# Kernel optimization log

Measured on AMD Instinct MI355X. Metric: run time of the kernel, lower is better.

Reference implementation:

```python
import jax, jax.numpy as jnp
import numpy as np

N_USERS = 100000
N_ITEMS = 50000
EMB_DIM = 64
N_LAYERS = 2
N_INTENTS = 128
N_EDGES = 4000000
N_NODES = N_USERS + N_ITEMS


def setup_inputs() -> dict:
    key = jax.random.key(0)
    k1, k2, k3, k4, k5 = jax.random.split(key, 5)
    return {
        "user_emb": 0.1 * jax.random.normal(k1, (N_USERS, EMB_DIM), dtype=jnp.float32),
        "item_emb": 0.1 * jax.random.normal(k2, (N_ITEMS, EMB_DIM), dtype=jnp.float32),
        "intents": jax.random.normal(k3, (EMB_DIM, N_INTENTS), dtype=jnp.float32) * (2.0 / (EMB_DIM + N_INTENTS)) ** 0.5,
        "h_idx": jax.random.randint(k4, (N_EDGES,), 0, N_NODES, dtype=jnp.int64)
        if jax.config.jax_enable_x64 else jax.random.randint(k4, (N_EDGES,), 0, N_NODES, dtype=jnp.int32),
        "t_idx": jax.random.randint(k5, (N_EDGES,), 0, N_NODES, dtype=jnp.int32),
    }


def _spmm(h_idx, t_idx, g_vals, x):
    # y[h] += g_vals * x[t]  (sparse matrix @ dense, COO form)
    gathered = x[t_idx] * g_vals[:, None]  # [E, D]
    return jax.ops.segment_sum(gathered, h_idx, num_segments=N_NODES)


def reference(user_emb, item_emb, intents, h_idx, t_idx):
    # --- _cal_sparse_adj: G = D^{-1/2} A D^{-1/2}, A values are ones ---
    deg = jax.ops.segment_sum(jnp.ones_like(h_idx, dtype=user_emb.dtype), h_idx,
                              num_segments=N_NODES)
    d_inv_sqrt = jnp.where(deg > 0, jax.lax.rsqrt(jnp.maximum(deg, 1e-12)), 0.0)
    g_vals = d_inv_sqrt[h_idx] * d_inv_sqrt[t_idx]  # [E]

    # --- multi-layer propagation with intent-aware embeddings ---
    embs = jnp.concatenate([user_emb, item_emb], axis=0)  # [N, D]
    all_embs = [embs]
    for _ in range(N_LAYERS):
        gnn_embs = _spmm(h_idx, t_idx, g_vals, embs)  # [N, D]
        # intent projection: softmax over intents, reconstruct in emb space
        u, it = embs[:N_USERS], embs[N_USERS:]
        u_int = jax.nn.softmax(u @ intents, axis=1) @ intents.T      # [n_users, D]
        i_int = jax.nn.softmax(it @ intents, axis=1) @ intents.T     # [n_items, D]
        int_embs = jnp.concatenate([u_int, i_int], axis=0)
        embs = gnn_embs + int_embs
        all_embs.append(embs)
    out = jnp.sum(jnp.stack(all_embs, axis=1), axis=1) / len(all_embs)  # mean over layers
    return out
```

## Files before the change

### kernel.cpp

```cpp
#include <hip/hip_runtime.h>
#include <math.h>

#define N_USERS 100000
#define N_ITEMS 50000
#define N_NODES 150000
#define EMB 64
#define NI 128
#define NUM_EDGES 4000000
#define NPAD 150016
#define NB 1172
#define BSTRIDE 4352
#define ETILE 8192
#define EGRID ((NUM_EDGES + ETILE - 1) / ETILE)
#define NT_ALL (NPAD / 16)
#define SBLK (NT_ALL / 4)
#define SENT 150000u

typedef __attribute__((ext_vector_type(8))) short bf16x8;
typedef __attribute__((ext_vector_type(4))) float f32x4;

__device__ __forceinline__ unsigned short f2bf(float f) {
    unsigned int u = __float_as_uint(f);
    u += 0x7FFFu + ((u >> 16) & 1u);
    return (unsigned short)(u >> 16);
}
__device__ __forceinline__ float bflo(unsigned int u) { return __uint_as_float(u << 16); }
__device__ __forceinline__ float bfhi(unsigned int u) { return __uint_as_float(u & 0xFFFF0000u); }


__global__ __launch_bounds__(512) void bucket_scatter(const int* __restrict__ h,
                                                      const int* __restrict__ t,
                                                      int* __restrict__ gcur,
                                                      unsigned int* __restrict__ ebuf) {
    __shared__ int lc[NB];
    __shared__ int lbase[NB];
    __shared__ int lcur[NB];
    int tid = threadIdx.x;
    for (int i = tid; i < NB; i += 512) lc[i] = 0;
    __syncthreads();
    int base = blockIdx.x * ETILE;
#pragma unroll
    for (int k = 0; k < ETILE / 512; ++k) {
        int idx = base + k * 512 + tid;
        if (idx < NUM_EDGES) atomicAdd(&lc[h[idx] >> 7], 1);
    }
    __syncthreads();
    for (int i = tid; i < NB; i += 512) {
        int c = lc[i];
        lbase[i] = c ? (i * BSTRIDE + atomicAdd(&gcur[i], c)) : 0;
        lcur[i] = 0;
    }
    __syncthreads();
#pragma unroll
    for (int k = 0; k < ETILE / 512; ++k) {
        int idx = base + k * 512 + tid;
        if (idx < NUM_EDGES) {
            int hh = h[idx], tt = t[idx];
            int b = hh >> 7;
            int p = lbase[b] + atomicAdd(&lcur[b], 1);
            int lim = b * BSTRIDE + BSTRIDE - 1;
            p = (p <= lim) ? p : lim;
            ebuf[p] = ((unsigned int)(hh & 127) << 18) | (unsigned int)tt;
        }
    }
}


__global__ __launch_bounds__(512) void bucket_csr(const int* __restrict__ gcur,
                                                  unsigned int* __restrict__ ebuf,
                                                  int2* __restrict__ rmeta,
                                                  float* __restrict__ dinv) {
    __shared__ unsigned int in_s[BSTRIDE];
    __shared__ int cnt_s[128];
    __shared__ int base_s[128];
    __shared__ int sc[128];
    int b = blockIdx.x, tid = threadIdx.x;
    int s = b * BSTRIDE;
    int n = gcur[b];
    if (n > BSTRIDE) n = BSTRIDE;

    for (int i = tid; i < n; i += 512) in_s[i] = ebuf[s + i];
    if (tid < 128) cnt_s[tid] = 0;
    __syncthreads();
    for (int i = tid; i < n; i += 512) atomicAdd(&cnt_s[in_s[i] >> 18], 1);
    __syncthreads();

    int c = 0, pc = 0;
    if (tid < 128) {
        c = cnt_s[tid];
        pc = (c + 3) & ~3;
        sc[tid] = pc;
    }
    __syncthreads();
    for (int off = 1; off < 128; off <<= 1) {
        int tv = 0;
        if (tid < 128 && tid >= off) tv = sc[tid - off];
        __syncthreads();
        if (tid < 128 && tid >= off) sc[tid] += tv;
        __syncthreads();
    }
    if (tid < 128) {
        int excl = sc[tid] - pc;
        base_s[tid] = excl;
        int node = (b << 7) + tid;
        rmeta[node] = make_int2(s + excl, pc);
        dinv[node] = (c > 0) ? rsqrtf((float)c) : 0.0f;
        for (int p2 = c; p2 < pc; ++p2) ebuf[s + excl + p2] = SENT;
        cnt_s[tid] = 0;
    }
    __syncthreads();
    for (int i = tid; i < n; i += 512) {
        unsigned int qv = in_s[i];
        int hl = (int)(qv >> 18);
        int p = base_s[hl] + atomicAdd(&cnt_s[hl], 1);
        ebuf[s + p] = qv & 0x3FFFFu;
    }
}


__global__ void init_kernel(const float4* __restrict__ ue4, const float4* __restrict__ ie4,
                            uint2* __restrict__ ebf4, float4* __restrict__ out4) {
    int i = blockIdx.x * blockDim.x + threadIdx.x;
    const int uelems = N_USERS * EMB / 4;
    const int relems = N_NODES * EMB / 4;
    const int total  = NPAD * EMB / 4;
    if (i < total) {
        float4 v = make_float4(0.f, 0.f, 0.f, 0.f);
        if (i < uelems) v = ue4[i];
        else if (i < relems) v = ie4[i - uelems];
        if (i < relems) out4[i] = v;
        unsigned int p0 = ((unsigned int)f2bf(v.y) << 16) | f2bf(v.x);
        unsigned int p1 = ((unsigned int)f2bf(v.w) << 16) | f2bf(v.z);
        ebf4[i] = make_uint2(p0, p1);
    }
}


__global__ __launch_bounds__(256) void wconv(const float* __restrict__ W,
                                             unsigned short* __restrict__ Wt,
                                             unsigned short* __restrict__ W2b) {
    int i = blockIdx.x * 256 + threadIdx.x;
    if (i < EMB * NI) {
        int d = i >> 7, c = i & 127;
        unsigned short b = f2bf(W[i]);
        W2b[i] = b;
        Wt[c * EMB + d] = b;
    }
}


__global__ __launch_bounds__(256, 6) void spmm_intent(const int2* __restrict__ rmeta,
                                                      const unsigned int* __restrict__ col,
                                                      const float* __restrict__ dinv,
                                                      const unsigned short* __restrict__ ebf,
                                                      unsigned short* __restrict__ ebfout,
                                                      const unsigned short* __restrict__ Wt,
                                                      const unsigned short* __restrict__ W2b,
                                                      float* __restrict__ acc, float scale) {
    __shared__ __align__(16) float UPool[4][1408];

    int tid = threadIdx.x;
    int wid = tid >> 6, lane = tid & 63;
    int q = lane >> 4, c = lane & 15;
    int qq = lane >> 3, cc = lane & 7;
    int tile = blockIdx.x * 4 + wid;
    if (tile >= NT_ALL) return;
    int rowbase = tile << 4;
    float* fw = &UPool[wid][0];
    unsigned short* pw = (unsigned short*)&UPool[wid][1088];

#pragma unroll 1
    for (int half = 0; half < 2; ++half) {
        int row = rowbase + half * 8 + qq;
        int2 rm = rmeta[row];
        int s = rm.x, pcv = rm.y;
        float dr = dinv[row];

        float a0 = 0.f, a1 = 0.f, a2 = 0.f, a3 = 0.f;
        float a4 = 0.f, a5 = 0.f, a6 = 0.f, a7 = 0.f;
        const unsigned short* eb = ebf + (cc << 3);

        uint4 cg0 = *(const uint4*)&col[s];
        int e0 = (int)(cg0.x & 0x3FFFFu), e1 = (int)(cg0.y & 0x3FFFFu);
        int e2 = (int)(cg0.z & 0x3FFFFu), e3 = (int)(cg0.w & 0x3FFFFu);
        float g0 = dinv[e0], g1 = dinv[e1], g2 = dinv[e2], g3 = dinv[e3];
        uint4 u0 = *(const uint4*)(eb + ((size_t)e0 << 6));
        uint4 u1 = *(const uint4*)(eb + ((size_t)e1 << 6));
        uint4 u2 = *(const uint4*)(eb + ((size_t)e2 << 6));
        uint4 u3 = *(const uint4*)(eb + ((size_t)e3 << 6));
        uint4 cg1 = *(const uint4*)&col[s + ((pcv >= 8) ? 4 : 0)];
        int f0 = (int)(cg1.x & 0x3FFFFu), f1 = (int)(cg1.y & 0x3FFFFu);
        int f2 = (int)(cg1.z & 0x3FFFFu), f3 = (int)(cg1.w & 0x3FFFFu);

        for (int it = 0; it < pcv; it += 4) {
            float h0 = dinv[f0], h1 = dinv[f1], h2 = dinv[f2], h3 = dinv[f3];
            uint4 v0 = *(const uint4*)(eb + ((size_t)f0 << 6));
            uint4 v1 = *(const uint4*)(eb + ((size_t)f1 << 6));
            uint4 v2 = *(const uint4*)(eb + ((size_t)f2 << 6));
            uint4 v3 = *(const uint4*)(eb + ((size_t)f3 << 6));
            int cb = s + it + 8;
            int ce = s + pcv - 4;
            uint4 cgn = *(const uint4*)&col[(cb < ce) ? cb : ce];
            __builtin_amdgcn_sched_barrier(0);
            a0 = fmaf(g0, bflo(u0.x), a0); a1 = fmaf(g0, bfhi(u0.x), a1);
            a2 = fmaf(g0, bflo(u0.y), a2); a3 = fmaf(g0, bfhi(u0.y), a3);
            a4 = fmaf(g0, bflo(u0.z), a4); a5 = fmaf(g0, bfhi(u0.z), a5);
            a6 = fmaf(g0, bflo(u0.w), a6); a7 = fmaf(g0, bfhi(u0.w), a7);
            a0 = fmaf(g1, bflo(u1.x), a0); a1 = fmaf(g1, bfhi(u1.x), a1);
            a2 = fmaf(g1, bflo(u1.y), a2); a3 = fmaf(g1, bfhi(u1.y), a3);
            a4 = fmaf(g1, bflo(u1.z), a4); a5 = fmaf(g1, bfhi(u1.z), a5);
            a6 = fmaf(g1, bflo(u1.w), a6); a7 = fmaf(g1, bfhi(u1.w), a7);
            a0 = fmaf(g2, bflo(u2.x), a0); a1 = fmaf(g2, bfhi(u2.x), a1);
            a2 = fmaf(g2, bflo(u2.y), a2); a3 = fmaf(g2, bfhi(u2.y), a3);
            a4 = fmaf(g2, bflo(u2.z), a4); a5 = fmaf(g2, bfhi(u2.z), a5);
            a6 = fmaf(g2, bflo(u2.w), a6); a7 = fmaf(g2, bfhi(u2.w), a7);
            a0 = fmaf(g3, bflo(u3.x), a0); a1 = fmaf(g3, bfhi(u3.x), a1);
            a2 = fmaf(g3, bflo(u3.y), a2); a3 = fmaf(g3, bfhi(u3.y), a3);
            a4 = fmaf(g3, bflo(u3.z), a4); a5 = fmaf(g3, bfhi(u3.z), a5);
            a6 = fmaf(g3, bflo(u3.w), a6); a7 = fmaf(g3, bfhi(u3.w), a7);
            u0 = v0; u1 = v1; u2 = v2; u3 = v3;
            g0 = h0; g1 = h1; g2 = h2; g3 = h3;
            f0 = (int)(cgn.x & 0x3FFFFu); f1 = (int)(cgn.y & 0x3FFFFu);
            f2 = (int)(cgn.z & 0x3FFFFu); f3 = (int)(cgn.w & 0x3FFFFu);
        }
        int fb = (half * 8 + qq) * 68 + (cc << 3);
        fw[fb + 0] = a0 * dr; fw[fb + 1] = a1 * dr;
        fw[fb + 2] = a2 * dr; fw[fb + 3] = a3 * dr;
        fw[fb + 4] = a4 * dr; fw[fb + 5] = a5 * dr;
        fw[fb + 6] = a6 * dr; fw[fb + 7] = a7 * dr;
    }

    const unsigned short* erow = ebf + ((size_t)(rowbase + c) << 6);
    bf16x8 A0 = *(const bf16x8*)(erow + (q << 3));
    bf16x8 A1 = *(const bf16x8*)(erow + 32 + (q << 3));
    f32x4 S[8];
#pragma unroll
    for (int t = 0; t < 8; ++t) {
        bf16x8 B0 = *(const bf16x8*)&Wt[(16 * t + c) * EMB + (q << 3)];
        bf16x8 B1 = *(const bf16x8*)&Wt[(16 * t + c) * EMB + 32 + (q << 3)];
        f32x4 z = {0.f, 0.f, 0.f, 0.f};
        z = __builtin_amdgcn_mfma_f32_16x16x32_bf16(A0, B0, z, 0, 0, 0);
        S[t] = __builtin_amdgcn_mfma_f32_16x16x32_bf16(A1, B1, z, 0, 0, 0);
    }

#pragma unroll
    for (int r = 0; r < 4; ++r) {
        float m = S[0][r];
#pragma unroll
        for (int t = 1; t < 8; ++t) m = fmaxf(m, S[t][r]);
        m = fmaxf(m, __shfl_xor(m, 1)); m = fmaxf(m, __shfl_xor(m, 2));
        m = fmaxf(m, __shfl_xor(m, 4)); m = fmaxf(m, __shfl_xor(m, 8));
        float sum = 0.f;
#pragma unroll
        for (int t = 0; t < 8; ++t) { float ex = __expf(S[t][r] - m); S[t][r] = ex; sum += ex; }
        sum += __shfl_xor(sum, 1); sum += __shfl_xor(sum, 2);
        sum += __shfl_xor(sum, 4); sum += __shfl_xor(sum, 8);
        float inv = 1.0f / sum;
#pragma unroll
        for (int t = 0; t < 8; ++t) S[t][r] *= inv;
    }

    f32x4 O0 = {0.f, 0.f, 0.f, 0.f}, O1 = O0, O2 = O0, O3 = O0;
#pragma unroll
    for (int s2 = 0; s2 < 4; ++s2) {
#pragma unroll
        for (int h2 = 0; h2 < 2; ++h2) {
            int t = 2 * s2 + h2;
#pragma unroll
            for (int r = 0; r < 4; ++r) {
                float p = S[t][r];
                unsigned short b = f2bf(p);
                pw[(4 * q + r) * 40 + (h2 << 4) + c] = b;
                S[t][r] = p - bflo((unsigned int)b);
            }
        }
        bf16x8 Pf = *(const bf16x8*)&pw[c * 40 + (q << 3)];
        {
            bf16x8 Bf0 = *(const bf16x8*)&W2b[(c) * NI + (s2 << 5) + (q << 3)];
            bf16x8 Bf1 = *(const bf16x8*)&W2b[(16 + c) * NI + (s2 << 5) + (q << 3)];
            O0 = __builtin_amdgcn_mfma_f32_16x16x32_bf16(Pf, Bf0, O0, 0, 0, 0);
            O1 = __builtin_amdgcn_mfma_f32_16x16x32_bf16(Pf, Bf1, O1, 0, 0, 0);
            bf16x8 Bf2 = *(const bf16x8*)&W2b[(32 + c) * NI + (s2 << 5) + (q << 3)];
            bf16x8 Bf3 = *(const bf16x8*)&W2b[(48 + c) * NI + (s2 << 5) + (q << 3)];
            O2 = __builtin_amdgcn_mfma_f32_16x16x32_bf16(Pf, Bf2, O2, 0, 0, 0);
            O3 = __builtin_amdgcn_mfma_f32_16x16x32_bf16(Pf, Bf3, O3, 0, 0, 0);
        }
#pragma unroll
        for (int h2 = 0; h2 < 2; ++h2) {
            int t = 2 * s2 + h2;
#pragma unroll
            for (int r = 0; r < 4; ++r)
                pw[(4 * q + r) * 40 + (h2 << 4) + c] = f2bf(S[t][r]);
        }
        bf16x8 Pl = *(const bf16x8*)&pw[c * 40 + (q << 3)];
        {
            bf16x8 Bf0 = *(const bf16x8*)&W2b[(c) * NI + (s2 << 5) + (q << 3)];
            bf16x8 Bf1 = *(const bf16x8*)&W2b[(16 + c) * NI + (s2 << 5) + (q << 3)];
            O0 = __builtin_amdgcn_mfma_f32_16x16x32_bf16(Pl, Bf0, O0, 0, 0, 0);
            O1 = __builtin_amdgcn_mfma_f32_16x16x32_bf16(Pl, Bf1, O1, 0, 0, 0);
            bf16x8 Bf2 = *(const bf16x8*)&W2b[(32 + c) * NI + (s2 << 5) + (q << 3)];
            bf16x8 Bf3 = *(const bf16x8*)&W2b[(48 + c) * NI + (s2 << 5) + (q << 3)];
            O2 = __builtin_amdgcn_mfma_f32_16x16x32_bf16(Pl, Bf2, O2, 0, 0, 0);
            O3 = __builtin_amdgcn_mfma_f32_16x16x32_bf16(Pl, Bf3, O3, 0, 0, 0);
        }
    }

    asm volatile("" ::: "memory");

#pragma unroll
    for (int r = 0; r < 4; ++r) {
        int rl = 4 * q + r;
        float* gr = &fw[rl * 68];
        gr[c]      += O0[r];
        gr[16 + c] += O1[r];
        gr[32 + c] += O2[r];
        gr[48 + c] += O3[r];
    }

    {
        int j = lane >> 2, sg = lane & 3;
        int rw = rowbase + j;
        const float* gr = &fw[j * 68 + (sg << 4)];
        float4 x0 = *(const float4*)&gr[0];
        float4 x1 = *(const float4*)&gr[4];
        float4 x2 = *(const float4*)&gr[8];
        float4 x3 = *(const float4*)&gr[12];
        size_t base = ((size_t)rw << 6) + (sg << 4);
        uint4 w0, w1;
        w0.x = (unsigned int)f2bf(x0.x) | ((unsigned int)f2bf(x0.y) << 16);
        w0.y = (unsigned int)f2bf(x0.z) | ((unsigned int)f2bf(x0.w) << 16);
        w0.z = (unsigned int)f2bf(x1.x) | ((unsigned int)f2bf(x1.y) << 16);
        w0.w = (unsigned int)f2bf(x1.z) | ((unsigned int)f2bf(x1.w) << 16);
        w1.x = (unsigned int)f2bf(x2.x) | ((unsigned int)f2bf(x2.y) << 16);
        w1.y = (unsigned int)f2bf(x2.z) | ((unsigned int)f2bf(x2.w) << 16);
        w1.z = (unsigned int)f2bf(x3.x) | ((unsigned int)f2bf(x3.y) << 16);
        w1.w = (unsigned int)f2bf(x3.z) | ((unsigned int)f2bf(x3.w) << 16);
        *(uint4*)(ebfout + base) = w0;
        *(uint4*)(ebfout + base + 8) = w1;
        if (rw < N_NODES) {
            float4* ap = (float4*)(acc + base);
            float4 b0 = ap[0], b1 = ap[1], b2 = ap[2], b3 = ap[3];
            b0.x = (b0.x + x0.x) * scale; b0.y = (b0.y + x0.y) * scale;
            b0.z = (b0.z + x0.z) * scale; b0.w = (b0.w + x0.w) * scale;
            b1.x = (b1.x + x1.x) * scale; b1.y = (b1.y + x1.y) * scale;
            b1.z = (b1.z + x1.z) * scale; b1.w = (b1.w + x1.w) * scale;
            b2.x = (b2.x + x2.x) * scale; b2.y = (b2.y + x2.y) * scale;
            b2.z = (b2.z + x2.z) * scale; b2.w = (b2.w + x2.w) * scale;
            b3.x = (b3.x + x3.x) * scale; b3.y = (b3.y + x3.y) * scale;
            b3.z = (b3.z + x3.z) * scale; b3.w = (b3.w + x3.w) * scale;
            ap[0] = b0; ap[1] = b1; ap[2] = b2; ap[3] = b3;
        }
    }
}


extern "C" void kernel_launch(void* const* d_in, const int* in_sizes, int n_in,
                              void* d_out, int out_size, void* d_ws, size_t ws_size,
                              hipStream_t stream) {
    const float* ue = (const float*)d_in[0];
    const float* ie = (const float*)d_in[1];
    const float* W  = (const float*)d_in[2];
    const int*   h  = (const int*)d_in[3];
    const int*   t  = (const int*)d_in[4];
    float* out = (float*)d_out;

    int*            gcur  = (int*)d_ws;
    int2*           rmeta = (int2*)(gcur + 2048);
    float*          dinv  = (float*)(rmeta + NPAD);
    unsigned short* ebfA  = (unsigned short*)(dinv + NPAD);
    unsigned short* ebfB  = ebfA + (size_t)NPAD * EMB;
    unsigned int*   ebuf  = (unsigned int*)(ebfB + (size_t)NPAD * EMB);
    unsigned short* Wt    = (unsigned short*)(ebuf + NB * BSTRIDE + 16);
    unsigned short* W2b   = Wt + EMB * NI;

    hipMemsetAsync(gcur, 0, NB * sizeof(int), stream);
    hipMemsetAsync(ebuf + NB * BSTRIDE, 0, 16 * sizeof(unsigned int), stream);
    bucket_scatter<<<EGRID, 512, 0, stream>>>(h, t, gcur, ebuf);
    bucket_csr<<<NB, 512, 0, stream>>>(gcur, ebuf, rmeta, dinv);
    init_kernel<<<(NPAD * EMB / 4 + 255) / 256, 256, 0, stream>>>(
        (const float4*)ue, (const float4*)ie, (uint2*)ebfA, (float4*)out);
    wconv<<<(EMB * NI + 255) / 256, 256, 0, stream>>>(W, Wt, W2b);

    const unsigned int* col = ebuf;
    spmm_intent<<<SBLK, 256, 0, stream>>>(rmeta, col, dinv, ebfA, ebfB, Wt, W2b, out, 1.0f);
    spmm_intent<<<SBLK, 256, 0, stream>>>(rmeta, col, dinv, ebfB, ebfA, Wt, W2b, out, 1.0f / 3.0f);
}
```

Before: 458.2 us.

## Stage neighbor indices and degree weights in LDS; per-wave bucket counters

The SpMM gather now loads up to 64 column indices per row into shared memory cooperatively across the 8 lanes of each row group. It also precomputes their dinv weights there with padding masked to zero, then issues 8 independent row gathers per iteration instead of the software-pipelined 4-wide loop. Rows with more than 64 entries fall back to a direct loop. The CSR bucket kernel splits its shared-memory histogram into per-wave copies to reduce atomic contention. Shared memory per block grows and the occupancy hint drops from 6 to 4 blocks, which trades latency hiding for wider per-thread memory-level parallelism.

Result: faster. 443.2 us (-3.3%).

```diff
diff --git a/kernel.cpp b/kernel.cpp
--- a/kernel.cpp
+++ b/kernel.cpp
@@ -71,23 +71,27 @@
                                                   int2* __restrict__ rmeta,
                                                   float* __restrict__ dinv) {
     __shared__ unsigned int in_s[BSTRIDE];
-    __shared__ int cnt_s[128];
+    __shared__ int cnt8[8][128];
+    __shared__ int wb8[8][128];
     __shared__ int base_s[128];
     __shared__ int sc[128];
-    int b = blockIdx.x, tid = threadIdx.x;
+    int b = blockIdx.x, tid = threadIdx.x, wid = tid >> 6;
     int s = b * BSTRIDE;
     int n = gcur[b];
     if (n > BSTRIDE) n = BSTRIDE;
 
     for (int i = tid; i < n; i += 512) in_s[i] = ebuf[s + i];
-    if (tid < 128) cnt_s[tid] = 0;
-    __syncthreads();
-    for (int i = tid; i < n; i += 512) atomicAdd(&cnt_s[in_s[i] >> 18], 1);
+    for (int i = tid; i < 1024; i += 512) ((int*)cnt8)[i] = 0;
+    __syncthreads();
+    for (int i = tid; i < n; i += 512) atomicAdd(&cnt8[wid][in_s[i] >> 18], 1);
     __syncthreads();
 
     int c = 0, pc = 0;
     if (tid < 128) {
-        c = cnt_s[tid];
+        int acc = 0;
+#pragma unroll
+        for (int w = 0; w < 8; ++w) { wb8[w][tid] = acc; acc += cnt8[w][tid]; }
+        c = acc;
         pc = (c + 3) & ~3;
         sc[tid] = pc;
     }
@@ -106,13 +110,14 @@
         rmeta[node] = make_int2(s + excl, pc);
         dinv[node] = (c > 0) ? rsqrtf((float)c) : 0.0f;
         for (int p2 = c; p2 < pc; ++p2) ebuf[s + excl + p2] = SENT;
-        cnt_s[tid] = 0;
-    }
+    }
+    __syncthreads();
+    for (int i = tid; i < 1024; i += 512) ((int*)cnt8)[i] = 0;
     __syncthreads();
     for (int i = tid; i < n; i += 512) {
         unsigned int qv = in_s[i];
         int hl = (int)(qv >> 18);
-        int p = base_s[hl] + atomicAdd(&cnt_s[hl], 1);
+        int p = base_s[hl] + wb8[wid][hl] + atomicAdd(&cnt8[wid][hl], 1);
         ebuf[s + p] = qv & 0x3FFFFu;
     }
 }
@@ -149,7 +154,7 @@
 }
 
 
-__global__ __launch_bounds__(256, 6) void spmm_intent(const int2* __restrict__ rmeta,
+__global__ __launch_bounds__(256, 4) void spmm_intent(const int2* __restrict__ rmeta,
                                                       const unsigned int* __restrict__ col,
                                                       const float* __restrict__ dinv,
                                                       const unsigned short* __restrict__ ebf,
@@ -157,7 +162,7 @@
                                                       const unsigned short* __restrict__ Wt,
                                                       const unsigned short* __restrict__ W2b,
                                                       float* __restrict__ acc, float scale) {
-    __shared__ __align__(16) float UPool[4][1408];
+    __shared__ __align__(16) float UPool[4][2496];
 
     int tid = threadIdx.x;
     int wid = tid >> 6, lane = tid & 63;
@@ -168,6 +173,8 @@
     int rowbase = tile << 4;
     float* fw = &UPool[wid][0];
     unsigned short* pw = (unsigned short*)&UPool[wid][1088];
+    unsigned int* cb = (unsigned int*)&UPool[wid][1408];
+    float* gb = &UPool[wid][1952];
 
 #pragma unroll 1
     for (int half = 0; half < 2; ++half) {
@@ -176,32 +183,93 @@
         int s = rm.x, pcv = rm.y;
         float dr = dinv[row];
 
+        {
+            int eoff = cc << 3;
+            uint4 c0 = *(const uint4*)&col[s + eoff];
+            uint4 c1 = *(const uint4*)&col[s + eoff + 4];
+            c0.x = (c0.x < NPAD) ? c0.x : (NPAD - 1);
+            c0.y = (c0.y < NPAD) ? c0.y : (NPAD - 1);
+            c0.z = (c0.z < NPAD) ? c0.z : (NPAD - 1);
+            c0.w = (c0.w < NPAD) ? c0.w : (NPAD - 1);
+            c1.x = (c1.x < NPAD) ? c1.x : (NPAD - 1);
+            c1.y = (c1.y < NPAD) ? c1.y : (NPAD - 1);
+            c1.z = (c1.z < NPAD) ? c1.z : (NPAD - 1);
+            c1.w = (c1.w < NPAD) ? c1.w : (NPAD - 1);
+            int lb = qq * 68 + eoff;
+            *(uint4*)&cb[lb]     = c0;
+            *(uint4*)&cb[lb + 4] = c1;
+            float g0 = dinv[c0.x], g1 = dinv[c0.y], g2 = dinv[c0.z], g3 = dinv[c0.w];
+            float g4 = dinv[c1.x], g5 = dinv[c1.y], g6 = dinv[c1.z], g7 = dinv[c1.w];
+            gb[lb + 0] = (eoff + 0 < pcv) ? g0 : 0.f;
+            gb[lb + 1] = (eoff + 1 < pcv) ? g1 : 0.f;
+            gb[lb + 2] = (eoff + 2 < pcv) ? g2 : 0.f;
+            gb[lb + 3] = (eoff + 3 < pcv) ? g3 : 0.f;
+            gb[lb + 4] = (eoff + 4 < pcv) ? g4 : 0.f;
+            gb[lb + 5] = (eoff + 5 < pcv) ? g5 : 0.f;
+            gb[lb + 6] = (eoff + 6 < pcv) ? g6 : 0.f;
+            gb[lb + 7] = (eoff + 7 < pcv) ? g7 : 0.f;
+        }
+
         float a0 = 0.f, a1 = 0.f, a2 = 0.f, a3 = 0.f;
         float a4 = 0.f, a5 = 0.f, a6 = 0.f, a7 = 0.f;
         const unsigned short* eb = ebf + (cc << 3);
-
-        uint4 cg0 = *(const uint4*)&col[s];
-        int e0 = (int)(cg0.x & 0x3FFFFu), e1 = (int)(cg0.y & 0x3FFFFu);
-        int e2 = (int)(cg0.z & 0x3FFFFu), e3 = (int)(cg0.w & 0x3FFFFu);
-        float g0 = dinv[e0], g1 = dinv[e1], g2 = dinv[e2], g3 = dinv[e3];
-        uint4 u0 = *(const uint4*)(eb + ((size_t)e0 << 6));
-        uint4 u1 = *(const uint4*)(eb + ((size_t)e1 << 6));
-        uint4 u2 = *(const uint4*)(eb + ((size_t)e2 << 6));
-        uint4 u3 = *(const uint4*)(eb + ((size_t)e3 << 6));
-        uint4 cg1 = *(const uint4*)&col[s + ((pcv >= 8) ? 4 : 0)];
-        int f0 = (int)(cg1.x & 0x3FFFFu), f1 = (int)(cg1.y & 0x3FFFFu);
-        int f2 = (int)(cg1.z & 0x3FFFFu), f3 = (int)(cg1.w & 0x3FFFFu);
-
-        for (int it = 0; it < pcv; it += 4) {
-            float h0 = dinv[f0], h1 = dinv[f1], h2 = dinv[f2], h3 = dinv[f3];
-            uint4 v0 = *(const uint4*)(eb + ((size_t)f0 << 6));
-            uint4 v1 = *(const uint4*)(eb + ((size_t)f1 << 6));
-            uint4 v2 = *(const uint4*)(eb + ((size_t)f2 << 6));
-            uint4 v3 = *(const uint4*)(eb + ((size_t)f3 << 6));
-            int cb = s + it + 8;
-            int ce = s + pcv - 4;
-            uint4 cgn = *(const uint4*)&col[(cb < ce) ? cb : ce];
-            __builtin_amdgcn_sched_barrier(0);
+        const unsigned int* cbr = &cb[qq * 68];
+        const float* gbr = &gb[qq * 68];
+        int lim = (pcv < 64) ? pcv : 64;
+
+        for (int it = 0; it < lim; it += 8) {
+            uint4 ca = *(const uint4*)&cbr[it];
+            uint4 cd = *(const uint4*)&cbr[it + 4];
+            float4 ga = *(const float4*)&gbr[it];
+            float4 gd = *(const float4*)&gbr[it + 4];
+            uint4 u0 = *(const uint4*)(eb + ((size_t)ca.x << 6));
+            uint4 u1 = *(const uint4*)(eb + ((size_t)ca.y << 6));
+            uint4 u2 = *(const uint4*)(eb + ((size_t)ca.z << 6));
+            uint4 u3 = *(const uint4*)(eb + ((size_t)ca.w << 6));
+            uint4 u4 = *(const uint4*)(eb + ((size_t)cd.x << 6));
+            uint4 u5 = *(const uint4*)(eb + ((size_t)cd.y << 6));
+            uint4 u6 = *(const uint4*)(eb + ((size_t)cd.z << 6));
+            uint4 u7 = *(const uint4*)(eb + ((size_t)cd.w << 6));
+            a0 = fmaf(ga.x, bflo(u0.x), a0); a1 = fmaf(ga.x, bfhi(u0.x), a1);
+            a2 = fmaf(ga.x, bflo(u0.y), a2); a3 = fmaf(ga.x, bfhi(u0.y), a3);
+            a4 = fmaf(ga.x, bflo(u0.z), a4); a5 = fmaf(ga.x, bfhi(u0.z), a5);
+            a6 = fmaf(ga.x, bflo(u0.w), a6); a7 = fmaf(ga.x, bfhi(u0.w), a7);
+            a0 = fmaf(ga.y, bflo(u1.x), a0); a1 = fmaf(ga.y, bfhi(u1.x), a1);
+            a2 = fmaf(ga.y, bflo(u1.y), a2); a3 = fmaf(ga.y, bfhi(u1.y), a3);
+            a4 = fmaf(ga.y, bflo(u1.z), a4); a5 = fmaf(ga.y, bfhi(u1.z), a5);
+            a6 = fmaf(ga.y, bflo(u1.w), a6); a7 = fmaf(ga.y, bfhi(u1.w), a7);
+            a0 = fmaf(ga.z, bflo(u2.x), a0); a1 = fmaf(ga.z, bfhi(u2.x), a1);
+            a2 = fmaf(ga.z, bflo(u2.y), a2); a3 = fmaf(ga.z, bfhi(u2.y), a3);
+            a4 = fmaf(ga.z, bflo(u2.z), a4); a5 = fmaf(ga.z, bfhi(u2.z), a5);
+            a6 = fmaf(ga.z, bflo(u2.w), a6); a7 = fmaf(ga.z, bfhi(u2.w), a7);
+            a0 = fmaf(ga.w, bflo(u3.x), a0); a1 = fmaf(ga.w, bfhi(u3.x), a1);
+            a2 = fmaf(ga.w, bflo(u3.y), a2); a3 = fmaf(ga.w, bfhi(u3.y), a3);
+            a4 = fmaf(ga.w, bflo(u3.z), a4); a5 = fmaf(ga.w, bfhi(u3.z), a5);
+            a6 = fmaf(ga.w, bflo(u3.w), a6); a7 = fmaf(ga.w, bfhi(u3.w), a7);
+            a0 = fmaf(gd.x, bflo(u4.x), a0); a1 = fmaf(gd.x, bfhi(u4.x), a1);
+            a2 = fmaf(gd.x, bflo(u4.y), a2); a3 = fmaf(gd.x, bfhi(u4.y), a3);
+            a4 = fmaf(gd.x, bflo(u4.z), a4); a5 = fmaf(gd.x, bfhi(u4.z), a5);
+            a6 = fmaf(gd.x, bflo(u4.w), a6); a7 = fmaf(gd.x, bfhi(u4.w), a7);
+            a0 = fmaf(gd.y, bflo(u5.x), a0); a1 = fmaf(gd.y, bfhi(u5.x), a1);
+            a2 = fmaf(gd.y, bflo(u5.y), a2); a3 = fmaf(gd.y, bfhi(u5.y), a3);
+            a4 = fmaf(gd.y, bflo(u5.z), a4); a5 = fmaf(gd.y, bfhi(u5.z), a5);
+            a6 = fmaf(gd.y, bflo(u5.w), a6); a7 = fmaf(gd.y, bfhi(u5.w), a7);
+            a0 = fmaf(gd.z, bflo(u6.x), a0); a1 = fmaf(gd.z, bfhi(u6.x), a1);
+            a2 = fmaf(gd.z, bflo(u6.y), a2); a3 = fmaf(gd.z, bfhi(u6.y), a3);
+            a4 = fmaf(gd.z, bflo(u6.z), a4); a5 = fmaf(gd.z, bfhi(u6.z), a5);
+            a6 = fmaf(gd.z, bflo(u6.w), a6); a7 = fmaf(gd.z, bfhi(u6.w), a7);
+            a0 = fmaf(gd.w, bflo(u7.x), a0); a1 = fmaf(gd.w, bfhi(u7.x), a1);
+            a2 = fmaf(gd.w, bflo(u7.y), a2); a3 = fmaf(gd.w, bfhi(u7.y), a3);
+            a4 = fmaf(gd.w, bflo(u7.z), a4); a5 = fmaf(gd.w, bfhi(u7.z), a5);
+            a6 = fmaf(gd.w, bflo(u7.w), a6); a7 = fmaf(gd.w, bfhi(u7.w), a7);
+        }
+        for (int it = 64; it < pcv; it += 4) {
+            uint4 cq = *(const uint4*)&col[s + it];
+            float g0 = dinv[cq.x], g1 = dinv[cq.y], g2 = dinv[cq.z], g3 = dinv[cq.w];
+            uint4 u0 = *(const uint4*)(eb + ((size_t)cq.x << 6));
+            uint4 u1 = *(const uint4*)(eb + ((size_t)cq.y << 6));
+            uint4 u2 = *(const uint4*)(eb + ((size_t)cq.z << 6));
+            uint4 u3 = *(const uint4*)(eb + ((size_t)cq.w << 6));
             a0 = fmaf(g0, bflo(u0.x), a0); a1 = fmaf(g0, bfhi(u0.x), a1);
             a2 = fmaf(g0, bflo(u0.y), a2); a3 = fmaf(g0, bfhi(u0.y), a3);
             a4 = fmaf(g0, bflo(u0.z), a4); a5 = fmaf(g0, bfhi(u0.z), a5);
@@ -218,10 +286,6 @@
             a2 = fmaf(g3, bflo(u3.y), a2); a3 = fmaf(g3, bfhi(u3.y), a3);
             a4 = fmaf(g3, bflo(u3.z), a4); a5 = fmaf(g3, bfhi(u3.z), a5);
             a6 = fmaf(g3, bflo(u3.w), a6); a7 = fmaf(g3, bfhi(u3.w), a7);
-            u0 = v0; u1 = v1; u2 = v2; u3 = v3;
-            g0 = h0; g1 = h1; g2 = h2; g3 = h3;
-            f0 = (int)(cgn.x & 0x3FFFFu); f1 = (int)(cgn.y & 0x3FFFFu);
-            f2 = (int)(cgn.z & 0x3FFFFu); f3 = (int)(cgn.w & 0x3FFFFu);
         }
         int fb = (half * 8 + qq) * 68 + (cc << 3);
         fw[fb + 0] = a0 * dr; fw[fb + 1] = a1 * dr;
```
